# Kernel optimization log

Hardware: AMD Instinct MI355X
Metric: run time of the kernel (lower is better)

Reference implementation:

```python
import jax, jax.numpy as jnp
import numpy as np

B, D, H, W = 4, 32, 32, 32
N_E = 32768


def setup_inputs() -> dict:
    key = jax.random.key(0)
    k1, k2 = jax.random.split(key)
    z = jax.random.normal(k1, (B, D, H, W), dtype=jnp.float32)
    embedding = jax.random.normal(k2, (N_E, D), dtype=jnp.float32)
    return {"z": z, "embedding": embedding}


def reference(z, embedding):
    # logits: [b, n, h, w] -- similarity of each spatial latent to every code
    logits = jnp.einsum('bdhw,nd->bnhw', z, embedding)
    ind = jnp.argmax(logits, axis=1)            # [b, h, w]
    z_q = embedding[ind]                        # [b, h, w, d]
    z_q = jnp.transpose(z_q, (0, 3, 1, 2))      # [b, d, h, w]
    return z_q, ind.reshape(-1)
```

## Files before the change

kernel.cpp:

```cpp
#include <hip/hip_runtime.h>
#include <math.h>

constexpr int Bc   = 4;
constexpr int Dc   = 32;
constexpr int HWc  = 1024;
constexpr int NE   = 32768;
constexpr int POS  = Bc * HWc;

constexpr int CCODES = 256;
constexpr int NCHUNK = NE / CCODES;
constexpr int PPB    = 512;
constexpr int NPBLK  = POS / PPB;

typedef _Float16 f16x8 __attribute__((ext_vector_type(8)));
typedef float    f32x4 __attribute__((ext_vector_type(4)));
typedef unsigned long long u64;

__device__ inline unsigned encF(float v) {
    unsigned u = __float_as_uint(v);
    return (u & 0x80000000u) ? ~u : (u | 0x80000000u);
}
__device__ inline u64 packVK(float v, int k) {
    return ((u64)encF(v) << 32) | (unsigned)(~k);
}

__global__ __launch_bounds__(256) void vq_eprep(
    const float* __restrict__ emb, const float* __restrict__ z,
    _Float16* __restrict__ Es, _Float16* __restrict__ Zs,
    u64* __restrict__ best2)
{
    float x[Dc];
    _Float16* dptr;
    if (blockIdx.x < NE / 256) {
        const int c = blockIdx.x * 256 + threadIdx.x;
        const float4* src = reinterpret_cast<const float4*>(emb + (size_t)c * Dc);
#pragma unroll
        for (int q = 0; q < 8; ++q) {
            const float4 v = src[q];
            x[4*q+0] = v.x; x[4*q+1] = v.y; x[4*q+2] = v.z; x[4*q+3] = v.w;
        }
        dptr = Es + (size_t)c * 64;
    } else {
        const int p = (blockIdx.x - NE / 256) * 256 + threadIdx.x;
        best2[p] = 0ULL;
        const int b = p >> 10, hw = p & (HWc - 1);
        const float* zp = z + (size_t)b * Dc * HWc + hw;
#pragma unroll
        for (int d = 0; d < Dc; ++d) x[d] = zp[(size_t)d * HWc];
        dptr = Zs + (size_t)p * 64;
    }
    f16x8* dst = reinterpret_cast<f16x8*>(dptr);
#pragma unroll
    for (int q = 0; q < 4; ++q) {
        f16x8 h, l;
#pragma unroll
        for (int r = 0; r < 8; ++r) {
            const float xv = x[8*q+r];
            const _Float16 hv = (_Float16)xv;
            h[r] = hv;
            l[r] = (_Float16)(xv - (float)hv);
        }
        dst[q]     = h;
        dst[4 + q] = l;
    }
}

__global__ __launch_bounds__(512)
__attribute__((amdgpu_waves_per_eu(4, 8)))
void vq_phaseA(
    const _Float16* __restrict__ Zs, const _Float16* __restrict__ Es,
    u64* __restrict__ best2)
{
    __shared__ __align__(16) char lds[PPB * 17 * 4];

    const int lin  = blockIdx.x;
    const int xcd  = lin & 7;
    const int j    = lin >> 3;
    const int chunk = xcd * (NCHUNK / 8) + (j & (NCHUNK / 8 - 1));
    const int pblk  = j >> 4;
    const int tid  = threadIdx.x;
    const int wave = tid >> 6, lane = tid & 63;
    const int m = lane & 15, g = lane >> 4;

    {
        const char* src = (const char*)(Es + (size_t)chunk * CCODES * 64);
        char* dstbase = lds + wave * 1024;
#pragma unroll
        for (int r = 0; r < 4; ++r) {
            const int o    = r * 512 + tid;
            const int row  = o >> 3;
            const int ccol = o & 7;
            const int soff = row * 128 + ((ccol ^ (row & 7)) << 4);
            __builtin_amdgcn_global_load_lds(
                (const __attribute__((address_space(1))) void*)(src + soff),
                (__attribute__((address_space(3))) void*)(dstbase + r * 8192),
                16, 0, 0);
        }
    }

    const int posBase0 = pblk * PPB;
    const int posBase  = posBase0 + wave * 64;
    f16x8 Ahi[4], Alo[4];
#pragma unroll
    for (int t = 0; t < 4; ++t) {
        const _Float16* zrow = Zs + (size_t)(posBase + t * 16 + m) * 64 + 8 * g;
        Ahi[t] = *reinterpret_cast<const f16x8*>(zrow);
        Alo[t] = *reinterpret_cast<const f16x8*>(zrow + 32);
    }
#pragma unroll
    for (int t = 0; t < 4; ++t) asm volatile("" : "+v"(Ahi[t]), "+v"(Alo[t]));

    f32x4 zacc = {0.f, 0.f, 0.f, 0.f};
    asm volatile("" : "+v"(zacc));

    float bval[16];
#pragma unroll
    for (int i = 0; i < 16; ++i) bval[i] = -INFINITY;

    __syncthreads();

    const char* lbase = lds;
    const int off_h = m * 128 + (( g      ^ (m & 7)) << 4);
    const int off_l = m * 128 + (((g + 4) ^ (m & 7)) << 4);

#pragma unroll 2
    for (int ct = 0; ct < CCODES / 16; ct += 2) {
        const char* p0 = lbase + ct * 2048;
        const f16x8 Bh0 = *reinterpret_cast<const f16x8*>(p0 + off_h);
        const f16x8 Bl0 = *reinterpret_cast<const f16x8*>(p0 + off_l);
        const f16x8 Bh1 = *reinterpret_cast<const f16x8*>(p0 + 2048 + off_h);
        const f16x8 Bl1 = *reinterpret_cast<const f16x8*>(p0 + 2048 + off_l);

#pragma unroll
        for (int t = 0; t < 4; ++t) {
            f32x4 aA, aB;
            aA = __builtin_amdgcn_mfma_f32_16x16x32_f16(Ahi[t], Bh0, zacc, 0, 0, 0);
            aB = __builtin_amdgcn_mfma_f32_16x16x32_f16(Ahi[t], Bh1, zacc, 0, 0, 0);
            aA = __builtin_amdgcn_mfma_f32_16x16x32_f16(Ahi[t], Bl0, aA,  0, 0, 0);
            aB = __builtin_amdgcn_mfma_f32_16x16x32_f16(Ahi[t], Bl1, aB,  0, 0, 0);
            aA = __builtin_amdgcn_mfma_f32_16x16x32_f16(Alo[t], Bh0, aA,  0, 0, 0);
            aB = __builtin_amdgcn_mfma_f32_16x16x32_f16(Alo[t], Bh1, aB,  0, 0, 0);
#pragma unroll
            for (int r = 0; r < 4; ++r)
                bval[t*4+r] = fmaxf(fmaxf(bval[t*4+r], aA[r]), aB[r]);
        }
    }

    __syncthreads();
    float* red = reinterpret_cast<float*>(lds);
#pragma unroll
    for (int i = 0; i < 16; ++i) {
        const int t = i >> 2, r = i & 3;
        const int row = wave * 64 + t * 16 + 4 * g + r;
        red[row * 17 + m] = bval[i];
    }
    __syncthreads();
    {
        float mx = red[tid * 17];
#pragma unroll
        for (int mm = 1; mm < 16; ++mm) mx = fmaxf(mx, red[tid * 17 + mm]);
        atomicMax(best2 + posBase0 + tid, packVK(mx, chunk));
    }
}

__global__ __launch_bounds__(256) void vq_phaseB(
    const float* __restrict__ z, const float* __restrict__ emb,
    const u64* __restrict__ best2, float* __restrict__ zq,
    float* __restrict__ indOut)
{
    const int p    = blockIdx.x * 4 + (threadIdx.x >> 6);
    const int lane = threadIdx.x & 63;

    const int chunk = (int)(~(unsigned)best2[p]) & (NCHUNK - 1);
    const int cbase = chunk * CCODES;
    const int b = p >> 10, hw = p & (HWc - 1);

    const int d0 = (lane & 7) * 4;
    const float* zp = z + (size_t)b * Dc * HWc + hw;
    const float z0 = zp[(size_t)(d0 + 0) * HWc];
    const float z1 = zp[(size_t)(d0 + 1) * HWc];
    const float z2 = zp[(size_t)(d0 + 2) * HWc];
    const float z3 = zp[(size_t)(d0 + 3) * HWc];

    const float4* eb = reinterpret_cast<const float4*>(emb + (size_t)cbase * Dc);

    float bv = -INFINITY;
    int   bi = cbase;
#pragma unroll 4
    for (int s = 0; s < 32; ++s) {
        const float4 ev = eb[s * 64 + lane];
        float d = z0 * ev.x + z1 * ev.y;
        d = fmaf(z2, ev.z, d);
        d = fmaf(z3, ev.w, d);
        d += __shfl_xor(d, 1, 64);
        d += __shfl_xor(d, 2, 64);
        d += __shfl_xor(d, 4, 64);
        const int code = cbase + s * 8 + (lane >> 3);
        const bool up = d > bv;
        bi = up ? code : bi;
        bv = fmaxf(bv, d);
    }

    u64 pk = packVK(bv, bi);
#pragma unroll
    for (int s = 8; s < 64; s <<= 1) {
        const u64 o = __shfl_xor(pk, s, 64);
        if (o > pk) pk = o;
    }
    const int widx = (int)(~(unsigned)pk);

    if (lane < Dc) {
        const float ev = emb[(size_t)widx * Dc + lane];
        zq[(size_t)b * Dc * HWc + (size_t)lane * HWc + hw] = ev;
    }
    if (lane == 0) indOut[p] = (float)widx;
}

__global__ __launch_bounds__(256, 4) void vq_scalar(
    const float* __restrict__ z, const float* __restrict__ emb,
    u64* __restrict__ best)
{
    const int lin = blockIdx.x;
    const int xcd = lin & 7, j = lin >> 3;
    const int seg    = xcd * 32 + (j & 31);
    const int posgrp = j >> 5;

    const int t  = posgrp * 256 + threadIdx.x;
    const int p0 = t, p1 = t + POS / 2;
    const int b0 = p0 >> 10, hw0 = p0 & (HWc - 1);
    const int b1 = p1 >> 10, hw1 = p1 & (HWc - 1);
    const float* zp0 = z + (size_t)b0 * Dc * HWc + hw0;
    const float* zp1 = z + (size_t)b1 * Dc * HWc + hw1;

    float za[Dc], zb[Dc];
#pragma unroll
    for (int d = 0; d < Dc; ++d) {
        za[d] = zp0[(size_t)d * HWc];
        zb[d] = zp1[(size_t)d * HWc];
    }
#pragma unroll
    for (int d = 0; d < Dc; ++d) asm volatile("" : "+v"(za[d]), "+v"(zb[d]));

    const int c0 = seg * 128;
    const float4* e4 = reinterpret_cast<const float4*>(emb + (size_t)c0 * Dc);
    float v0 = -INFINITY, v1 = -INFINITY;
    int   i0 = c0, i1 = c0;
#pragma unroll 1
    for (int cc = 0; cc < 128; ++cc, e4 += 8) {
        float a0 = 0.f, a1 = 0.f;
#pragma unroll
        for (int q = 0; q < 8; ++q) {
            const float4 e = e4[q];
            a0 = fmaf(za[4*q+0], e.x, a0); a1 = fmaf(zb[4*q+0], e.x, a1);
            a0 = fmaf(za[4*q+1], e.y, a0); a1 = fmaf(zb[4*q+1], e.y, a1);
            a0 = fmaf(za[4*q+2], e.z, a0); a1 = fmaf(zb[4*q+2], e.z, a1);
            a0 = fmaf(za[4*q+3], e.w, a0); a1 = fmaf(zb[4*q+3], e.w, a1);
        }
        const int c = c0 + cc;
        if (a0 > v0) { v0 = a0; i0 = c; }
        if (a1 > v1) { v1 = a1; i1 = c; }
    }
    atomicMax(best + p0, packVK(v0, i0));
    atomicMax(best + p1, packVK(v1, i1));
}

__global__ __launch_bounds__(256) void vq_finish_kernel(
    const u64* __restrict__ best, const float* __restrict__ emb,
    float* __restrict__ zq, float* __restrict__ indOut)
{
    const int p = blockIdx.x * 256 + threadIdx.x;
    const int idx = (int)(~(unsigned)best[p]);

    const float4* e = reinterpret_cast<const float4*>(emb + (size_t)idx * Dc);
    const int b  = p >> 10;
    const int hw = p & (HWc - 1);
    float* o = zq + (size_t)b * Dc * HWc + hw;
#pragma unroll
    for (int q = 0; q < 8; ++q) {
        const float4 v = e[q];
        o[(size_t)(4*q+0) * HWc] = v.x;
        o[(size_t)(4*q+1) * HWc] = v.y;
        o[(size_t)(4*q+2) * HWc] = v.z;
        o[(size_t)(4*q+3) * HWc] = v.w;
    }
    indOut[p] = (float)idx;
}

extern "C" void kernel_launch(void* const* d_in, const int* in_sizes, int n_in,
                              void* d_out, int out_size, void* d_ws, size_t ws_size,
                              hipStream_t stream)
{
    const float* z   = (const float*)d_in[0];
    const float* emb = (const float*)d_in[1];

    float* out    = (float*)d_out;
    float* zq     = out;
    float* indOut = out + (size_t)Bc * Dc * HWc;

    char* w = (char*)d_ws;
    u64*      best2 = (u64*)w;          w += (size_t)POS * 8;
    _Float16* Es    = (_Float16*)w;     w += (size_t)NE * 64 * 2;
    _Float16* Zs    = (_Float16*)w;
    const size_t needed = (size_t)POS * 8 + (size_t)(NE + POS) * 64 * 2;

    if (ws_size >= needed) {
        hipLaunchKernelGGL(vq_eprep, dim3(NE / 256 + POS / 256), dim3(256), 0,
                           stream, emb, z, Es, Zs, best2);
        hipLaunchKernelGGL(vq_phaseA, dim3(NCHUNK * NPBLK), dim3(512), 0,
                           stream, Zs, Es, best2);
        hipLaunchKernelGGL(vq_phaseB, dim3(POS / 4), dim3(256), 0, stream,
                           z, emb, best2, zq, indOut);
    } else {
        hipMemsetAsync(best2, 0, (size_t)POS * sizeof(u64), stream);
        hipLaunchKernelGGL(vq_scalar, dim3(2048), dim3(256), 0, stream,
                           z, emb, best2);
        hipLaunchKernelGGL(vq_finish_kernel, dim3(POS / 256), dim3(256), 0,
                           stream, best2, emb, zq, indOut);
    }
}
```

Before: 41.24 us.

## Fuse fp16 split conversion into phaseA and replace atomics with per-chunk max table

Removes the separate prep kernel. PhaseA now loads fp32 embeddings straight into LDS and converts them in place to hi/lo fp16, and it converts z from global memory in registers. Instead of packed atomicMax into a per-position best, each block writes its chunk maximum into a position-by-chunk table. PhaseB then reduces the 128 chunk maxima per position with wave shuffles, which drops the memset/init and the atomic contention. The costs are a larger workspace, strided global z loads inside phaseA, and an extra LDS conversion pass plus barrier.

```diff
diff --git a/kernel.cpp b/kernel.cpp
--- a/kernel.cpp
+++ b/kernel.cpp
@@ -24,52 +24,11 @@
     return ((u64)encF(v) << 32) | (unsigned)(~k);
 }
 
-__global__ __launch_bounds__(256) void vq_eprep(
-    const float* __restrict__ emb, const float* __restrict__ z,
-    _Float16* __restrict__ Es, _Float16* __restrict__ Zs,
-    u64* __restrict__ best2)
-{
-    float x[Dc];
-    _Float16* dptr;
-    if (blockIdx.x < NE / 256) {
-        const int c = blockIdx.x * 256 + threadIdx.x;
-        const float4* src = reinterpret_cast<const float4*>(emb + (size_t)c * Dc);
-#pragma unroll
-        for (int q = 0; q < 8; ++q) {
-            const float4 v = src[q];
-            x[4*q+0] = v.x; x[4*q+1] = v.y; x[4*q+2] = v.z; x[4*q+3] = v.w;
-        }
-        dptr = Es + (size_t)c * 64;
-    } else {
-        const int p = (blockIdx.x - NE / 256) * 256 + threadIdx.x;
-        best2[p] = 0ULL;
-        const int b = p >> 10, hw = p & (HWc - 1);
-        const float* zp = z + (size_t)b * Dc * HWc + hw;
-#pragma unroll
-        for (int d = 0; d < Dc; ++d) x[d] = zp[(size_t)d * HWc];
-        dptr = Zs + (size_t)p * 64;
-    }
-    f16x8* dst = reinterpret_cast<f16x8*>(dptr);
-#pragma unroll
-    for (int q = 0; q < 4; ++q) {
-        f16x8 h, l;
-#pragma unroll
-        for (int r = 0; r < 8; ++r) {
-            const float xv = x[8*q+r];
-            const _Float16 hv = (_Float16)xv;
-            h[r] = hv;
-            l[r] = (_Float16)(xv - (float)hv);
-        }
-        dst[q]     = h;
-        dst[4 + q] = l;
-    }
-}
-
 __global__ __launch_bounds__(512)
 __attribute__((amdgpu_waves_per_eu(4, 8)))
 void vq_phaseA(
-    const _Float16* __restrict__ Zs, const _Float16* __restrict__ Es,
-    u64* __restrict__ best2)
+    const float* __restrict__ z, const float* __restrict__ emb,
+    unsigned* __restrict__ pcmax)
 {
     __shared__ __align__(16) char lds[PPB * 17 * 4];
 
@@ -83,7 +42,7 @@
     const int m = lane & 15, g = lane >> 4;
 
     {
-        const char* src = (const char*)(Es + (size_t)chunk * CCODES * 64);
+        const char* src = (const char*)(emb + (size_t)chunk * CCODES * Dc);
         char* dstbase = lds + wave * 1024;
 #pragma unroll
         for (int r = 0; r < 4; ++r) {
@@ -103,9 +62,16 @@
     f16x8 Ahi[4], Alo[4];
 #pragma unroll
     for (int t = 0; t < 4; ++t) {
-        const _Float16* zrow = Zs + (size_t)(posBase + t * 16 + m) * 64 + 8 * g;
-        Ahi[t] = *reinterpret_cast<const f16x8*>(zrow);
-        Alo[t] = *reinterpret_cast<const f16x8*>(zrow + 32);
+        const int pos = posBase + t * 16 + m;
+        const int b = pos >> 10, hw = pos & (HWc - 1);
+        const float* zp = z + (size_t)b * Dc * HWc + hw;
+#pragma unroll
+        for (int q = 0; q < 8; ++q) {
+            const float xv = zp[(size_t)(8 * g + q) * HWc];
+            const _Float16 hv = (_Float16)xv;
+            Ahi[t][q] = hv;
+            Alo[t][q] = (_Float16)(xv - (float)hv);
+        }
     }
 #pragma unroll
     for (int t = 0; t < 4; ++t) asm volatile("" : "+v"(Ahi[t]), "+v"(Alo[t]));
@@ -117,6 +83,32 @@
 #pragma unroll
     for (int i = 0; i < 16; ++i) bval[i] = -INFINITY;
 
+    __syncthreads();
+
+    if (tid < 256) {
+        char* myrow = lds + tid * 128;
+        float4 raw[8];
+#pragma unroll
+        for (int c = 0; c < 8; ++c)
+            raw[c] = *reinterpret_cast<const float4*>(myrow + ((c ^ (tid & 7)) << 4));
+        f16x8 h[4], l[4];
+#pragma unroll
+        for (int cc = 0; cc < 4; ++cc) {
+            const float4 a = raw[2 * cc], bq = raw[2 * cc + 1];
+            const float xs[8] = {a.x, a.y, a.z, a.w, bq.x, bq.y, bq.z, bq.w};
+#pragma unroll
+            for (int r = 0; r < 8; ++r) {
+                const _Float16 hv = (_Float16)xs[r];
+                h[cc][r] = hv;
+                l[cc][r] = (_Float16)(xs[r] - (float)hv);
+            }
+        }
+#pragma unroll
+        for (int cc = 0; cc < 4; ++cc) {
+            *reinterpret_cast<f16x8*>(myrow + (( cc      ^ (tid & 7)) << 4)) = h[cc];
+            *reinterpret_cast<f16x8*>(myrow + (((cc + 4) ^ (tid & 7)) << 4)) = l[cc];
+        }
+    }
     __syncthreads();
 
     const char* lbase = lds;
@@ -159,19 +151,29 @@
         float mx = red[tid * 17];
 #pragma unroll
         for (int mm = 1; mm < 16; ++mm) mx = fmaxf(mx, red[tid * 17 + mm]);
-        atomicMax(best2 + posBase0 + tid, packVK(mx, chunk));
+        pcmax[(size_t)(posBase0 + tid) * NCHUNK + chunk] = encF(mx);
     }
 }
 
 __global__ __launch_bounds__(256) void vq_phaseB(
     const float* __restrict__ z, const float* __restrict__ emb,
-    const u64* __restrict__ best2, float* __restrict__ zq,
+    const unsigned* __restrict__ pcmax, float* __restrict__ zq,
     float* __restrict__ indOut)
 {
     const int p    = blockIdx.x * 4 + (threadIdx.x >> 6);
     const int lane = threadIdx.x & 63;
 
-    const int chunk = (int)(~(unsigned)best2[p]) & (NCHUNK - 1);
+    const unsigned v0 = pcmax[(size_t)p * NCHUNK + lane];
+    const unsigned v1 = pcmax[(size_t)p * NCHUNK + 64 + lane];
+    u64 pk0 = ((u64)v0 << 32) | (unsigned)(~lane);
+    u64 pk1 = ((u64)v1 << 32) | (unsigned)(~(64 + lane));
+    u64 pk = pk0 > pk1 ? pk0 : pk1;
+#pragma unroll
+    for (int s = 1; s < 64; s <<= 1) {
+        const u64 o = __shfl_xor(pk, s, 64);
+        if (o > pk) pk = o;
+    }
+    const int chunk = (int)(~(unsigned)pk) & (NCHUNK - 1);
     const int cbase = chunk * CCODES;
     const int b = p >> 10, hw = p & (HWc - 1);
 
@@ -201,13 +203,13 @@
         bv = fmaxf(bv, d);
     }
 
-    u64 pk = packVK(bv, bi);
+    u64 pki = packVK(bv, bi);
 #pragma unroll
     for (int s = 8; s < 64; s <<= 1) {
-        const u64 o = __shfl_xor(pk, s, 64);
-        if (o > pk) pk = o;
-    }
-    const int widx = (int)(~(unsigned)pk);
+        const u64 o = __shfl_xor(pki, s, 64);
+        if (o > pki) pki = o;
+    }
+    const int widx = (int)(~(unsigned)pki);
 
     if (lane < Dc) {
         const float ev = emb[(size_t)widx * Dc + lane];
@@ -297,24 +299,20 @@
     float* zq     = out;
     float* indOut = out + (size_t)Bc * Dc * HWc;
 
-    char* w = (char*)d_ws;
-    u64*      best2 = (u64*)w;          w += (size_t)POS * 8;
-    _Float16* Es    = (_Float16*)w;     w += (size_t)NE * 64 * 2;
-    _Float16* Zs    = (_Float16*)w;
-    const size_t needed = (size_t)POS * 8 + (size_t)(NE + POS) * 64 * 2;
+    unsigned* pcmax = (unsigned*)d_ws;
+    const size_t needed = (size_t)POS * NCHUNK * sizeof(unsigned);
 
     if (ws_size >= needed) {
-        hipLaunchKernelGGL(vq_eprep, dim3(NE / 256 + POS / 256), dim3(256), 0,
-                           stream, emb, z, Es, Zs, best2);
         hipLaunchKernelGGL(vq_phaseA, dim3(NCHUNK * NPBLK), dim3(512), 0,
-                           stream, Zs, Es, best2);
+                           stream, z, emb, pcmax);
         hipLaunchKernelGGL(vq_phaseB, dim3(POS / 4), dim3(256), 0, stream,
-                           z, emb, best2, zq, indOut);
+                           z, emb, pcmax, zq, indOut);
     } else {
-        hipMemsetAsync(best2, 0, (size_t)POS * sizeof(u64), stream);
+        u64* best = (u64*)d_ws;
+        hipMemsetAsync(best, 0, (size_t)POS * sizeof(u64), stream);
         hipLaunchKernelGGL(vq_scalar, dim3(2048), dim3(256), 0, stream,
-                           z, emb, best2);
+                           z, emb, best);
         hipLaunchKernelGGL(vq_finish_kernel, dim3(POS / 256), dim3(256), 0,
-                           stream, best2, emb, zq, indOut);
-    }
-}
+                           stream, best, emb, zq, indOut);
+    }
+}
```

Result: faster. 37.32 us (-9.5%).
